# Performance work log

Hardware: AMD Instinct MI355X
Metric: run time of the kernel (lower is better)

Reference implementation:

```python
import jax, jax.numpy as jnp
import numpy as np

H, DH = 16, 64          # num_heads, dim_head
DIM = 1024              # dim_ltn
EPS = 1e-5


def setup_inputs() -> dict:
    key = jax.random.key(0)
    ks = jax.random.split(key, 8)
    b, n_txt, t, m = 2, 2048, 4, 256
    text = jax.random.normal(ks[0], (b, n_txt, DIM), dtype=jnp.float32)
    image = jax.random.normal(ks[1], (b, t, m, DIM), dtype=jnp.float32)
    locations = jax.random.randint(ks[2], (b, n_txt), 0, 2)  # 0/1 media markers
    s = DIM ** -0.5
    Wq = jax.random.normal(ks[3], (DIM, H * DH), dtype=jnp.float32) * s
    Wkv = jax.random.normal(ks[4], (DIM, 2 * H * DH), dtype=jnp.float32) * s
    Wo = jax.random.normal(ks[5], (H * DH, DIM), dtype=jnp.float32) * s
    ln_gamma = jnp.ones((DIM,), dtype=jnp.float32)
    ln_beta = jnp.zeros((DIM,), dtype=jnp.float32)
    return {"text": text, "image": image, "locations": locations,
            "Wq": Wq, "Wkv": Wkv, "Wo": Wo,
            "ln_gamma": ln_gamma, "ln_beta": ln_beta}


def reference(text, image, locations, Wq, Wkv, Wo, ln_gamma, ln_beta):
    scale = DH ** -0.5
    b, t, m, d = image.shape
    # LayerNorm(text)
    mu = text.mean(-1, keepdims=True)
    var = ((text - mu) ** 2).mean(-1, keepdims=True)
    tn = (text - mu) / jnp.sqrt(var + EPS) * ln_gamma + ln_beta
    img = image.reshape(b, t * m, d)             # b (t m) d
    q = tn @ Wq                                  # b n (h dh)
    k, v = jnp.split(img @ Wkv, 2, axis=-1)      # each b tm (h dh)
    split_heads = lambda x: x.reshape(x.shape[0], x.shape[1], H, DH).transpose(0, 2, 1, 3)
    q, k, v = split_heads(q), split_heads(k), split_heads(v)
    attn = jnp.einsum('bhid,bhjd->bhij', q, k) * scale   # b h n (t m)
    txt_time = jnp.cumsum(locations, axis=-1)            # b n : media index per text token
    viz_time = jnp.repeat(jnp.arange(1, t + 1), m)       # (t m)
    # only_attend_to_immediate -> equality mask
    mask = txt_time[:, None, :, None] == viz_time[None, None, None, :]
    neg = -jnp.finfo(attn.dtype).max
    attn = jnp.where(mask, attn, neg)
    attn = jax.nn.softmax(attn, axis=-1)
    # zero attention for text tokens before any media (txt_time == 0)
    attn = jnp.where((txt_time == 0)[:, None, :, None], 0.0, attn)
    out = jnp.einsum('bhij,bhjd->bhid', attn, v)
    out = out.transpose(0, 2, 1, 3).reshape(b, -1, H * DH)
    return out @ Wo
```

## Files before the change

### kernel.cpp

```cpp
#include <hip/hip_runtime.h>

#define BATCH 2
#define NTXT  2048
#define TMED  4
#define MMED  256
#define TM    (TMED * MMED)
#define DIM   1024
#define NH    16
#define DHD   64
#define KVW   2048
#define RMAX  256
#define RT    32

typedef _Float16 f16x8 __attribute__((ext_vector_type(8)));
typedef float    f32x4 __attribute__((ext_vector_type(4)));

__global__ __launch_bounds__(1024) void scan_kernel(const int* __restrict__ loc,
                                                    int* __restrict__ tt,
                                                    int* __restrict__ seg) {
  __shared__ int buf[NTXT];
  __shared__ int s_start, s_end;
  const int b = blockIdx.x;
  const int tid = threadIdx.x;
  if (tid == 0) { s_start = NTXT; s_end = NTXT; }
  buf[tid]        = loc[b * NTXT + tid];
  buf[tid + 1024] = loc[b * NTXT + tid + 1024];
  __syncthreads();
  for (int off = 1; off < NTXT; off <<= 1) {
    int a0 = (tid >= off) ? buf[tid - off] : 0;
    int a1 = buf[tid + 1024 - off];
    __syncthreads();
    buf[tid] += a0;
    buf[tid + 1024] += a1;
    __syncthreads();
  }
  const int v0 = buf[tid], v1 = buf[tid + 1024];
  tt[b * NTXT + tid]        = v0;
  tt[b * NTXT + tid + 1024] = v1;
  if (v0 >= 1) atomicMin(&s_start, tid);
  if (v0 >= 5) atomicMin(&s_end, tid);
  if (v1 >= 1) atomicMin(&s_start, tid + 1024);
  if (v1 >= 5) atomicMin(&s_end, tid + 1024);
  __syncthreads();
  if (tid == 0) {
    seg[b * 2]     = s_start;
    seg[b * 2 + 1] = s_end - s_start;
  }
}

__global__ __launch_bounds__(256) void convert_kernel(const float* __restrict__ Wkv,
                                                      _Float16* __restrict__ Bt) {
  const int tb = blockIdx.x;
  const int k0 = (tb & 15) * 64, n0 = (tb >> 4) * 64;
  __shared__ float tile[64][65];
  const int tid = threadIdx.x;
  const int r = tid >> 4, c4 = (tid & 15) * 4;
#pragma unroll
  for (int i = 0; i < 4; i++) {
    const float4 v = *reinterpret_cast<const float4*>(
        Wkv + (size_t)(k0 + r + i * 16) * KVW + n0 + c4);
    tile[r + i * 16][c4 + 0] = v.x; tile[r + i * 16][c4 + 1] = v.y;
    tile[r + i * 16][c4 + 2] = v.z; tile[r + i * 16][c4 + 3] = v.w;
  }
  __syncthreads();
#pragma unroll
  for (int it = 0; it < 2; it++) {
    const int chunk = it * 256 + tid;
    const int n = chunk >> 3, kc = (chunk & 7) * 8;
    f16x8 h;
#pragma unroll
    for (int j = 0; j < 8; j++) h[j] = (_Float16)tile[kc + j][n];
    *reinterpret_cast<f16x8*>(Bt + (size_t)(n0 + n) * DIM + k0 + kc) = h;
  }
}

__global__ __launch_bounds__(512) void gemm_f16_kernel(
    const float* __restrict__ A, const _Float16* __restrict__ Bt,
    float* __restrict__ C, float* __restrict__ vbar) {
  const int M = BATCH * TM, N = KVW, K = DIM;
  (void)M;
  __shared__ _Float16 As[128 * 32];
  __shared__ _Float16 Bs[128 * 32];
  const int tid = threadIdx.x;
  const int lane = tid & 63, wid = tid >> 6;
  const int wm = wid & 3, wn = wid >> 2;
  const int row0 = blockIdx.y * 128, col0 = blockIdx.x * 128;
  const int srow = tid >> 2, skc = (tid & 3) * 8;
  const int frow = lane & 15, fq = lane >> 4;

  f32x4 acc[2][4] = {};

  for (int k0 = 0; k0 < K; k0 += 32) {
    const float* ap = A + (size_t)(row0 + srow) * K + k0 + skc;
    const float4 a0 = *reinterpret_cast<const float4*>(ap);
    const float4 a1 = *reinterpret_cast<const float4*>(ap + 4);
    f16x8 av;
    av[0] = (_Float16)a0.x; av[1] = (_Float16)a0.y;
    av[2] = (_Float16)a0.z; av[3] = (_Float16)a0.w;
    av[4] = (_Float16)a1.x; av[5] = (_Float16)a1.y;
    av[6] = (_Float16)a1.z; av[7] = (_Float16)a1.w;
    const f16x8 bv = *reinterpret_cast<const f16x8*>(
        Bt + (size_t)(col0 + srow) * K + k0 + skc);
    __syncthreads();
    *reinterpret_cast<f16x8*>(As + tid * 8) = av;
    *reinterpret_cast<f16x8*>(Bs + tid * 8) = bv;
    __syncthreads();

    f16x8 af[2], bf[4];
#pragma unroll
    for (int mt = 0; mt < 2; mt++)
      af[mt] = *reinterpret_cast<const f16x8*>(
          As + (wm * 32 + mt * 16 + frow) * 32 + fq * 8);
#pragma unroll
    for (int nt = 0; nt < 4; nt++)
      bf[nt] = *reinterpret_cast<const f16x8*>(
          Bs + (wn * 64 + nt * 16 + frow) * 32 + fq * 8);
#pragma unroll
    for (int mt = 0; mt < 2; mt++)
#pragma unroll
      for (int nt = 0; nt < 4; nt++)
        acc[mt][nt] = __builtin_amdgcn_mfma_f32_16x16x32_f16(
            af[mt], bf[nt], acc[mt][nt], 0, 0, 0);
  }

#pragma unroll
  for (int mt = 0; mt < 2; mt++)
#pragma unroll
    for (int nt = 0; nt < 4; nt++) {
      const int col = col0 + wn * 64 + nt * 16 + frow;
#pragma unroll
      for (int r = 0; r < 4; r++) {
        const int row = row0 + wm * 32 + mt * 16 + fq * 4 + r;
        C[(size_t)row * N + col] = acc[mt][nt][r];
      }
    }

  if (col0 >= DIM) {
    const int b = row0 >> 10;
#pragma unroll
    for (int nt = 0; nt < 4; nt++) {
      float s = 0.f;
#pragma unroll
      for (int mt = 0; mt < 2; mt++)
#pragma unroll
        for (int r = 0; r < 4; r++) s += acc[mt][nt][r];
      s += __shfl_down(s, 32);
      s += __shfl_down(s, 16);
      if (lane < 16)
        atomicAdd(&vbar[b * DIM + (col0 - DIM) + wn * 64 + nt * 16 + lane],
                  s * (1.0f / (float)TM));
    }
  }
}

__global__ __launch_bounds__(256) void obar_kernel(const float* __restrict__ vbar,
                                                   const float* __restrict__ Wo,
                                                   float* __restrict__ obar) {
  const int be = blockIdx.x;
  const int b = be >> 2, et = be & 3;
  const int ct = blockIdx.y;
  const int tid = threadIdx.x;
  float s = 0.f;
  const float* w = Wo + (size_t)(ct * 128) * DIM + et * 256 + tid;
  const float* vb = vbar + b * DIM + ct * 128;
  for (int c = 0; c < 128; c++) s += vb[c] * w[(size_t)c * DIM];
  atomicAdd(&obar[b * DIM + et * 256 + tid], s);
}

__global__ __launch_bounds__(256) void fill_kernel(
    const float* __restrict__ text, const float* __restrict__ kv,
    const float* __restrict__ Wq, const float* __restrict__ Wo,
    const float* __restrict__ gamma, const float* __restrict__ beta,
    const int* __restrict__ tt, const int* __restrict__ seg,
    const float* __restrict__ obar, float* __restrict__ out) {
  const int tid = threadIdx.x;
  const int b = blockIdx.x >> 11;
  const int i = blockIdx.x & (NTXT - 1);
  const int t = tt[b * NTXT + i];
  float* orow = out + (size_t)(b * NTXT + i) * DIM;

  if (t == 0) {
    for (int c = tid; c < DIM; c += 256) orow[c] = 0.f;
    return;
  }
  if (t > TMED) {
    const float* ob = obar + b * DIM;
    for (int c = tid; c < DIM; c += 256) orow[c] = ob[c];
    return;
  }
  if (i - seg[b * 2] < RMAX) return;

  __shared__ float tn[DIM];
  __shared__ float qrow[DIM];
  __shared__ float oaccs[DIM];
  __shared__ float red[256];
  __shared__ float pbuf[256];
  const float* xrow = text + (size_t)(b * NTXT + i) * DIM;
  float x[4];
  float s = 0.f;
#pragma unroll
  for (int u = 0; u < 4; u++) { x[u] = xrow[tid + 256 * u]; s += x[u]; }
  red[tid] = s; __syncthreads();
  for (int st = 128; st > 0; st >>= 1) {
    if (tid < st) red[tid] += red[tid + st];
    __syncthreads();
  }
  const float mu = red[0] * (1.0f / DIM); __syncthreads();
  float vs = 0.f;
#pragma unroll
  for (int u = 0; u < 4; u++) { float d = x[u] - mu; vs += d * d; }
  red[tid] = vs; __syncthreads();
  for (int st = 128; st > 0; st >>= 1) {
    if (tid < st) red[tid] += red[tid + st];
    __syncthreads();
  }
  const float rstd = rsqrtf(red[0] * (1.0f / DIM) + 1e-5f); __syncthreads();
#pragma unroll
  for (int u = 0; u < 4; u++) {
    const int c = tid + 256 * u;
    tn[c] = (x[u] - mu) * rstd * gamma[c] + beta[c];
  }
  __syncthreads();
  {
    float qa[4] = {0.f, 0.f, 0.f, 0.f};
    for (int c = 0; c < DIM; c++) {
      const float tv = tn[c];
      const float* w = Wq + (size_t)c * DIM + tid;
#pragma unroll
      for (int u = 0; u < 4; u++) qa[u] += tv * w[256 * u];
    }
#pragma unroll
    for (int u = 0; u < 4; u++) qrow[tid + 256 * u] = qa[u];
  }
  __syncthreads();
  const size_t kvrow0 = (size_t)(b * TM + (t - 1) * MMED) * KVW;
  const int d0 = tid & 63, g = tid >> 6;
  for (int h = 0; h < NH; h++) {
    const float* krow = kv + kvrow0 + (size_t)tid * KVW + h * DHD;
    float sc = 0.f;
#pragma unroll
    for (int d = 0; d < DHD; d++) sc += qrow[h * DHD + d] * krow[d];
    sc *= 0.125f;
    red[tid] = sc; __syncthreads();
    for (int st = 128; st > 0; st >>= 1) {
      if (tid < st) red[tid] = fmaxf(red[tid], red[tid + st]);
      __syncthreads();
    }
    const float mx = red[0]; __syncthreads();
    const float e = __expf(sc - mx);
    red[tid] = e; __syncthreads();
    for (int st = 128; st > 0; st >>= 1) {
      if (tid < st) red[tid] += red[tid + st];
      __syncthreads();
    }
    const float inv = 1.0f / red[0]; __syncthreads();
    pbuf[tid] = e * inv; __syncthreads();
    const float* vbase = kv + kvrow0 + (size_t)(g * 64) * KVW + DIM + h * DHD + d0;
    float a = 0.f;
#pragma unroll 8
    for (int j = 0; j < 64; j++) a += pbuf[g * 64 + j] * vbase[(size_t)j * KVW];
    red[tid] = a; __syncthreads();
    if (tid < 64)
      oaccs[h * DHD + tid] = red[tid] + red[64 + tid] + red[128 + tid] + red[192 + tid];
    __syncthreads();
  }
  float oa[4] = {0.f, 0.f, 0.f, 0.f};
  for (int c = 0; c < DIM; c++) {
    const float ov = oaccs[c];
    const float* w = Wo + (size_t)c * DIM + tid;
#pragma unroll
    for (int u = 0; u < 4; u++) oa[u] += ov * w[256 * u];
  }
#pragma unroll
  for (int u = 0; u < 4; u++) orow[tid + 256 * u] = oa[u];
}

__global__ __launch_bounds__(256) void attnh_kernel(
    const float* __restrict__ text, const float* __restrict__ kv,
    const float* __restrict__ Wq, const float* __restrict__ gamma,
    const float* __restrict__ beta, const int* __restrict__ tt,
    const int* __restrict__ seg, float* __restrict__ oacc) {
  const int h = blockIdx.x;
  const int rt = blockIdx.y;
  const int b = blockIdx.z;
  const int i0 = seg[b * 2];
  const int cnt = min(seg[b * 2 + 1], RMAX);
  const int tid = threadIdx.x;
  const int d0 = tid & 63, g = tid >> 6;
  __shared__ float tn_s[DIM];
  __shared__ float q[DHD];
  __shared__ float qp[4][DHD];
  __shared__ float red[256];
  __shared__ float pbuf[256];
  for (int r = rt; r < cnt; r += RT) {
    const int i = i0 + r;
    const int t = tt[b * NTXT + i];
    const float* xrow = text + (size_t)(b * NTXT + i) * DIM;
    float x[4];
    float s = 0.f;
#pragma unroll
    for (int u = 0; u < 4; u++) { x[u] = xrow[tid + 256 * u]; s += x[u]; }
    red[tid] = s; __syncthreads();
    for (int st = 128; st > 0; st >>= 1) {
      if (tid < st) red[tid] += red[tid + st];
      __syncthreads();
    }
    const float mu = red[0] * (1.0f / DIM); __syncthreads();
    float vs = 0.f;
#pragma unroll
    for (int u = 0; u < 4; u++) { float d = x[u] - mu; vs += d * d; }
    red[tid] = vs; __syncthreads();
    for (int st = 128; st > 0; st >>= 1) {
      if (tid < st) red[tid] += red[tid + st];
      __syncthreads();
    }
    const float rstd = rsqrtf(red[0] * (1.0f / DIM) + 1e-5f); __syncthreads();
#pragma unroll
    for (int u = 0; u < 4; u++) {
      const int c = tid + 256 * u;
      tn_s[c] = (x[u] - mu) * rstd * gamma[c] + beta[c];
    }
    __syncthreads();
    float qa = 0.f;
    const float* wq = Wq + (size_t)(g * 256) * DIM + h * DHD + d0;
    for (int c = 0; c < 256; c++) qa += tn_s[g * 256 + c] * wq[(size_t)c * DIM];
    qp[g][d0] = qa; __syncthreads();
    if (tid < 64) q[tid] = qp[0][tid] + qp[1][tid] + qp[2][tid] + qp[3][tid];
    __syncthreads();
    const size_t kvrow0 = (size_t)(b * TM + (t - 1) * MMED) * KVW;
    const float* krow = kv + kvrow0 + (size_t)tid * KVW + h * DHD;
    float sc = 0.f;
#pragma unroll
    for (int d = 0; d < DHD; d += 4) {
      const float4 kk = *reinterpret_cast<const float4*>(&krow[d]);
      sc += q[d] * kk.x + q[d + 1] * kk.y + q[d + 2] * kk.z + q[d + 3] * kk.w;
    }
    sc *= 0.125f;
    red[tid] = sc; __syncthreads();
    for (int st = 128; st > 0; st >>= 1) {
      if (tid < st) red[tid] = fmaxf(red[tid], red[tid + st]);
      __syncthreads();
    }
    const float mx = red[0]; __syncthreads();
    const float e = __expf(sc - mx);
    red[tid] = e; __syncthreads();
    for (int st = 128; st > 0; st >>= 1) {
      if (tid < st) red[tid] += red[tid + st];
      __syncthreads();
    }
    const float inv = 1.0f / red[0]; __syncthreads();
    pbuf[tid] = e * inv; __syncthreads();
    const float* vbase = kv + kvrow0 + (size_t)(g * 64) * KVW + DIM + h * DHD + d0;
    float a = 0.f;
#pragma unroll 8
    for (int j = 0; j < 64; j++) a += pbuf[g * 64 + j] * vbase[(size_t)j * KVW];
    red[tid] = a; __syncthreads();
    if (tid < 64)
      oacc[(size_t)(b * RMAX + r) * DIM + h * DHD + tid] =
          red[tid] + red[64 + tid] + red[128 + tid] + red[192 + tid];
    __syncthreads();
  }
}

__global__ __launch_bounds__(256) void oproj_kernel(
    const float* __restrict__ oacc, const float* __restrict__ Wo,
    const int* __restrict__ seg, float* __restrict__ out) {
  const int ct = blockIdx.x;
  const int rt = blockIdx.y;
  const int b = blockIdx.z;
  const int i0 = seg[b * 2];
  const int cnt = min(seg[b * 2 + 1], RMAX);
  const int tid = threadIdx.x;
  const int d0 = tid & 63, g = tid >> 6;
  __shared__ float op[4][64];
  for (int r = rt; r < cnt; r += RT) {
    const float* arow = oacc + (size_t)(b * RMAX + r) * DIM;
    const float* wo = Wo + (size_t)(g * 256) * DIM + ct * 64 + d0;
    float s = 0.f;
    for (int c = 0; c < 256; c++) s += arow[g * 256 + c] * wo[(size_t)c * DIM];
    op[g][d0] = s; __syncthreads();
    if (tid < 64)
      out[(size_t)(b * NTXT + i0 + r) * DIM + ct * 64 + tid] =
          op[0][tid] + op[1][tid] + op[2][tid] + op[3][tid];
    __syncthreads();
  }
}

extern "C" void kernel_launch(void* const* d_in, const int* in_sizes, int n_in,
                              void* d_out, int out_size, void* d_ws, size_t ws_size,
                              hipStream_t stream) {
  const float* text  = (const float*)d_in[0];
  const float* image = (const float*)d_in[1];
  const int*   loc   = (const int*)d_in[2];
  const float* Wq    = (const float*)d_in[3];
  const float* Wkv   = (const float*)d_in[4];
  const float* Wo    = (const float*)d_in[5];
  const float* gamma = (const float*)d_in[6];
  const float* beta  = (const float*)d_in[7];
  float* out = (float*)d_out;

  float*    kv   = (float*)d_ws;
  _Float16* WkvT = (_Float16*)(kv + (size_t)BATCH * TM * KVW);
  float*    oacc = (float*)WkvT;
  float*    vbar = (float*)(WkvT + (size_t)KVW * DIM);
  float*    obar = vbar + BATCH * DIM;
  int*      tt   = (int*)(obar + BATCH * DIM);
  int*      seg  = tt + BATCH * NTXT;

  scan_kernel<<<BATCH, 1024, 0, stream>>>(loc, tt, seg);
  convert_kernel<<<512, 256, 0, stream>>>(Wkv, WkvT);
  hipMemsetAsync(vbar, 0, 2 * BATCH * DIM * sizeof(float), stream);

  dim3 ggrid(KVW / 128, (BATCH * TM) / 128);
  gemm_f16_kernel<<<ggrid, 512, 0, stream>>>(image, WkvT, kv, vbar);

  obar_kernel<<<dim3(BATCH * 4, 8), 256, 0, stream>>>(vbar, Wo, obar);
  fill_kernel<<<BATCH * NTXT, 256, 0, stream>>>(text, kv, Wq, Wo, gamma, beta,
                                                tt, seg, obar, out);
  attnh_kernel<<<dim3(NH, RT, BATCH), 256, 0, stream>>>(text, kv, Wq, gamma,
                                                        beta, tt, seg, oacc);
  oproj_kernel<<<dim3(16, RT, BATCH), 256, 0, stream>>>(oacc, Wo, seg, out);
}
```

Measured before the change: 178.9 us.

## Merge kernels into five heterogeneous launches, store KV in fp16, precompute q

Replaces the eight-step launch sequence with five kernels that each carry several independent jobs, selected by block index: scan plus image-mean, weight transpose plus LayerNorm plus vbar, then GEMM plus q projection plus obar, then fill plus attention. The K/V projection output is now written as fp16, which halves the workspace traffic for the GEMM output and the attention reads. vbar is computed from the image mean times Wkv instead of through atomics in the GEMM epilogue. The aim is to cut launch gaps and memory traffic, at the cost of extra fp16 rounding in K/V and some idle or imbalanced blocks in the mixed-role kernels.

```diff
diff --git a/kernel.cpp b/kernel.cpp
--- a/kernel.cpp
+++ b/kernel.cpp
@@ -15,286 +15,260 @@
 typedef _Float16 f16x8 __attribute__((ext_vector_type(8)));
 typedef float    f32x4 __attribute__((ext_vector_type(4)));
 
-__global__ __launch_bounds__(1024) void scan_kernel(const int* __restrict__ loc,
-                                                    int* __restrict__ tt,
-                                                    int* __restrict__ seg) {
+__global__ __launch_bounds__(1024) void k1_scan_ibar(
+    const int* __restrict__ loc, const float* __restrict__ image,
+    int* __restrict__ tt, int* __restrict__ seg, float* __restrict__ ibar) {
   __shared__ int buf[NTXT];
   __shared__ int s_start, s_end;
-  const int b = blockIdx.x;
+  const int idx = blockIdx.x;
   const int tid = threadIdx.x;
-  if (tid == 0) { s_start = NTXT; s_end = NTXT; }
-  buf[tid]        = loc[b * NTXT + tid];
-  buf[tid + 1024] = loc[b * NTXT + tid + 1024];
-  __syncthreads();
-  for (int off = 1; off < NTXT; off <<= 1) {
-    int a0 = (tid >= off) ? buf[tid - off] : 0;
-    int a1 = buf[tid + 1024 - off];
-    __syncthreads();
-    buf[tid] += a0;
-    buf[tid + 1024] += a1;
-    __syncthreads();
+  if (idx < BATCH) {
+    const int b = idx;
+    if (tid == 0) { s_start = NTXT; s_end = NTXT; }
+    buf[tid]        = loc[b * NTXT + tid];
+    buf[tid + 1024] = loc[b * NTXT + tid + 1024];
+    __syncthreads();
+    for (int off = 1; off < NTXT; off <<= 1) {
+      int a0 = (tid >= off) ? buf[tid - off] : 0;
+      int a1 = buf[tid + 1024 - off];
+      __syncthreads();
+      buf[tid] += a0;
+      buf[tid + 1024] += a1;
+      __syncthreads();
+    }
+    const int v0 = buf[tid], v1 = buf[tid + 1024];
+    tt[b * NTXT + tid]        = v0;
+    tt[b * NTXT + tid + 1024] = v1;
+    if (v0 >= 1) atomicMin(&s_start, tid);
+    if (v0 >= 5) atomicMin(&s_end, tid);
+    if (v1 >= 1) atomicMin(&s_start, tid + 1024);
+    if (v1 >= 5) atomicMin(&s_end, tid + 1024);
+    __syncthreads();
+    if (tid == 0) {
+      seg[b * 2]     = s_start;
+      seg[b * 2 + 1] = s_end - s_start;
+    }
+  } else {
+    const int j = idx - BATCH;
+    const int b = j >> 3, rt = j & 7;
+    const float* p = image + (size_t)(b * TM + rt * 128) * DIM + tid;
+    float s = 0.f;
+#pragma unroll 4
+    for (int r = 0; r < 128; r++) s += p[(size_t)r * DIM];
+    atomicAdd(&ibar[b * DIM + tid], s * (1.0f / (float)TM));
   }
-  const int v0 = buf[tid], v1 = buf[tid + 1024];
-  tt[b * NTXT + tid]        = v0;
-  tt[b * NTXT + tid + 1024] = v1;
-  if (v0 >= 1) atomicMin(&s_start, tid);
-  if (v0 >= 5) atomicMin(&s_end, tid);
-  if (v1 >= 1) atomicMin(&s_start, tid + 1024);
-  if (v1 >= 5) atomicMin(&s_end, tid + 1024);
-  __syncthreads();
-  if (tid == 0) {
-    seg[b * 2]     = s_start;
-    seg[b * 2 + 1] = s_end - s_start;
+}
+
+__global__ __launch_bounds__(256) void k2_prep(
+    const float* __restrict__ Wkv, const float* __restrict__ text,
+    const float* __restrict__ gamma, const float* __restrict__ beta,
+    const int* __restrict__ seg, const float* __restrict__ ibar,
+    _Float16* __restrict__ WkvT, float* __restrict__ tn,
+    float* __restrict__ vbar) {
+  __shared__ float tile[64][65];
+  __shared__ float red[256];
+  const int idx = blockIdx.x;
+  const int tid = threadIdx.x;
+  if (idx < 512) {
+    const int k0 = (idx & 15) * 64, n0 = (idx >> 4) * 64;
+    const int r = tid >> 4, c4 = (tid & 15) * 4;
+#pragma unroll
+    for (int i = 0; i < 4; i++) {
+      const float4 v = *reinterpret_cast<const float4*>(
+          Wkv + (size_t)(k0 + r + i * 16) * KVW + n0 + c4);
+      tile[r + i * 16][c4 + 0] = v.x; tile[r + i * 16][c4 + 1] = v.y;
+      tile[r + i * 16][c4 + 2] = v.z; tile[r + i * 16][c4 + 3] = v.w;
+    }
+    __syncthreads();
+#pragma unroll
+    for (int it = 0; it < 2; it++) {
+      const int chunk = it * 256 + tid;
+      const int n = chunk >> 3, kc = (chunk & 7) * 8;
+      f16x8 h;
+#pragma unroll
+      for (int j = 0; j < 8; j++) h[j] = (_Float16)tile[kc + j][n];
+      *reinterpret_cast<f16x8*>(WkvT + (size_t)(n0 + n) * DIM + k0 + kc) = h;
+    }
+  } else if (idx < 576) {
+    const int j = idx - 512;
+    const int b = j >> 5, rt = j & 31;
+    const int i0 = seg[b * 2];
+    const int cnt = min(seg[b * 2 + 1], RMAX);
+    for (int r = rt; r < cnt; r += RT) {
+      const float* xrow = text + (size_t)(b * NTXT + i0 + r) * DIM;
+      float x[4];
+      float s = 0.f;
+#pragma unroll
+      for (int u = 0; u < 4; u++) { x[u] = xrow[tid + 256 * u]; s += x[u]; }
+      red[tid] = s; __syncthreads();
+      for (int st = 128; st > 0; st >>= 1) {
+        if (tid < st) red[tid] += red[tid + st];
+        __syncthreads();
+      }
+      const float mu = red[0] * (1.0f / DIM); __syncthreads();
+      float vs = 0.f;
+#pragma unroll
+      for (int u = 0; u < 4; u++) { float d = x[u] - mu; vs += d * d; }
+      red[tid] = vs; __syncthreads();
+      for (int st = 128; st > 0; st >>= 1) {
+        if (tid < st) red[tid] += red[tid + st];
+        __syncthreads();
+      }
+      const float rstd = rsqrtf(red[0] * (1.0f / DIM) + 1e-5f); __syncthreads();
+      float* trow = tn + (size_t)(b * RMAX + r) * DIM;
+#pragma unroll
+      for (int u = 0; u < 4; u++) {
+        const int c = tid + 256 * u;
+        trow[c] = (x[u] - mu) * rstd * gamma[c] + beta[c];
+      }
+      __syncthreads();
+    }
+  } else {
+    const int j = idx - 576;
+    const int b = j >> 2, et = j & 3;
+    const int e = et * 256 + tid;
+    const float* vb = ibar + b * DIM;
+    float s = 0.f;
+    for (int c = 0; c < DIM; c++) s += vb[c] * Wkv[(size_t)c * KVW + DIM + e];
+    vbar[b * DIM + e] = s;
   }
 }
 
-__global__ __launch_bounds__(256) void convert_kernel(const float* __restrict__ Wkv,
-                                                      _Float16* __restrict__ Bt) {
-  const int tb = blockIdx.x;
-  const int k0 = (tb & 15) * 64, n0 = (tb >> 4) * 64;
-  __shared__ float tile[64][65];
+__global__ __launch_bounds__(512) void k3_gemm_qproj_obar(
+    const float* __restrict__ image, const _Float16* __restrict__ WkvT,
+    const float* __restrict__ Wq, const float* __restrict__ Wo,
+    const float* __restrict__ tn, const float* __restrict__ vbar,
+    const int* __restrict__ seg, _Float16* __restrict__ kv16,
+    float* __restrict__ qbuf, float* __restrict__ obar) {
+  __shared__ char smem[49152];
+  const int idx = blockIdx.x;
   const int tid = threadIdx.x;
-  const int r = tid >> 4, c4 = (tid & 15) * 4;
-#pragma unroll
-  for (int i = 0; i < 4; i++) {
-    const float4 v = *reinterpret_cast<const float4*>(
-        Wkv + (size_t)(k0 + r + i * 16) * KVW + n0 + c4);
-    tile[r + i * 16][c4 + 0] = v.x; tile[r + i * 16][c4 + 1] = v.y;
-    tile[r + i * 16][c4 + 2] = v.z; tile[r + i * 16][c4 + 3] = v.w;
+  if (idx < 256) {
+    _Float16* As = (_Float16*)smem;
+    _Float16* Bs = As + 128 * 32;
+    const int lane = tid & 63, wid = tid >> 6;
+    const int wm = wid & 3, wn = wid >> 2;
+    const int row0 = (idx >> 4) * 128, col0 = (idx & 15) * 128;
+    const int srow = tid >> 2, skc = (tid & 3) * 8;
+    const int frow = lane & 15, fq = lane >> 4;
+    f32x4 acc[2][4] = {};
+    for (int k0 = 0; k0 < DIM; k0 += 32) {
+      const float* ap = image + (size_t)(row0 + srow) * DIM + k0 + skc;
+      const float4 a0 = *reinterpret_cast<const float4*>(ap);
+      const float4 a1 = *reinterpret_cast<const float4*>(ap + 4);
+      f16x8 av;
+      av[0] = (_Float16)a0.x; av[1] = (_Float16)a0.y;
+      av[2] = (_Float16)a0.z; av[3] = (_Float16)a0.w;
+      av[4] = (_Float16)a1.x; av[5] = (_Float16)a1.y;
+      av[6] = (_Float16)a1.z; av[7] = (_Float16)a1.w;
+      const f16x8 bv = *reinterpret_cast<const f16x8*>(
+          WkvT + (size_t)(col0 + srow) * DIM + k0 + skc);
+      __syncthreads();
+      *reinterpret_cast<f16x8*>(As + tid * 8) = av;
+      *reinterpret_cast<f16x8*>(Bs + tid * 8) = bv;
+      __syncthreads();
+      f16x8 af[2], bf[4];
+#pragma unroll
+      for (int mt = 0; mt < 2; mt++)
+        af[mt] = *reinterpret_cast<const f16x8*>(
+            As + (wm * 32 + mt * 16 + frow) * 32 + fq * 8);
+#pragma unroll
+      for (int nt = 0; nt < 4; nt++)
+        bf[nt] = *reinterpret_cast<const f16x8*>(
+            Bs + (wn * 64 + nt * 16 + frow) * 32 + fq * 8);
+#pragma unroll
+      for (int mt = 0; mt < 2; mt++)
+#pragma unroll
+        for (int nt = 0; nt < 4; nt++)
+          acc[mt][nt] = __builtin_amdgcn_mfma_f32_16x16x32_f16(
+              af[mt], bf[nt], acc[mt][nt], 0, 0, 0);
+    }
+#pragma unroll
+    for (int mt = 0; mt < 2; mt++)
+#pragma unroll
+      for (int nt = 0; nt < 4; nt++) {
+        const int col = col0 + wn * 64 + nt * 16 + frow;
+#pragma unroll
+        for (int r = 0; r < 4; r++) {
+          const int row = row0 + wm * 32 + mt * 16 + fq * 4 + r;
+          kv16[(size_t)row * KVW + col] = (_Float16)acc[mt][nt][r];
+        }
+      }
+  } else if (idx < 272) {
+    float* tn_s = (float*)smem;
+    float* qred = tn_s + 8 * 1024;
+    const int j = idx - 256;
+    const int b = j >> 3, nt = j & 7;
+    const int n0 = nt * 128;
+    const int d0 = tid & 127, g = tid >> 7;
+    const int cnt = min(seg[b * 2 + 1], RMAX);
+    for (int r0 = 0; r0 < cnt; r0 += 8) {
+      const float* src = tn + (size_t)(b * RMAX + r0) * DIM;
+      for (int i = tid; i < 8 * 1024; i += 512) tn_s[i] = src[i];
+      __syncthreads();
+      float acc[8] = {};
+      const float* wq = Wq + (size_t)(g * 256) * DIM + n0 + d0;
+      for (int c = 0; c < 256; c++) {
+        const float w = wq[(size_t)c * DIM];
+#pragma unroll
+        for (int rr = 0; rr < 8; rr++)
+          acc[rr] += tn_s[rr * 1024 + g * 256 + c] * w;
+      }
+#pragma unroll
+      for (int rr = 0; rr < 8; rr++) qred[(g * 8 + rr) * 128 + d0] = acc[rr];
+      __syncthreads();
+      if (g == 0) {
+#pragma unroll
+        for (int rr = 0; rr < 8; rr++) {
+          if (r0 + rr < cnt) {
+            const float s = qred[rr * 128 + d0] + qred[(8 + rr) * 128 + d0] +
+                            qred[(16 + rr) * 128 + d0] + qred[(24 + rr) * 128 + d0];
+            qbuf[(size_t)(b * RMAX + r0 + rr) * DIM + n0 + d0] = s;
+          }
+        }
+      }
+      __syncthreads();
+    }
+  } else {
+    const int j = idx - 272;
+    const int b = j >> 1, et = j & 1;
+    const int e = et * 512 + tid;
+    const float* vb = vbar + b * DIM;
+    float s = 0.f;
+    for (int c = 0; c < DIM; c++) s += vb[c] * Wo[(size_t)c * DIM + e];
+    obar[b * DIM + e] = s;
   }
-  __syncthreads();
-#pragma unroll
-  for (int it = 0; it < 2; it++) {
-    const int chunk = it * 256 + tid;
-    const int n = chunk >> 3, kc = (chunk & 7) * 8;
-    f16x8 h;
-#pragma unroll
-    for (int j = 0; j < 8; j++) h[j] = (_Float16)tile[kc + j][n];
-    *reinterpret_cast<f16x8*>(Bt + (size_t)(n0 + n) * DIM + k0 + kc) = h;
-  }
-}
-
-__global__ __launch_bounds__(512) void gemm_f16_kernel(
-    const float* __restrict__ A, const _Float16* __restrict__ Bt,
-    float* __restrict__ C, float* __restrict__ vbar) {
-  const int M = BATCH * TM, N = KVW, K = DIM;
-  (void)M;
-  __shared__ _Float16 As[128 * 32];
-  __shared__ _Float16 Bs[128 * 32];
-  const int tid = threadIdx.x;
-  const int lane = tid & 63, wid = tid >> 6;
-  const int wm = wid & 3, wn = wid >> 2;
-  const int row0 = blockIdx.y * 128, col0 = blockIdx.x * 128;
-  const int srow = tid >> 2, skc = (tid & 3) * 8;
-  const int frow = lane & 15, fq = lane >> 4;
-
-  f32x4 acc[2][4] = {};
-
-  for (int k0 = 0; k0 < K; k0 += 32) {
-    const float* ap = A + (size_t)(row0 + srow) * K + k0 + skc;
-    const float4 a0 = *reinterpret_cast<const float4*>(ap);
-    const float4 a1 = *reinterpret_cast<const float4*>(ap + 4);
-    f16x8 av;
-    av[0] = (_Float16)a0.x; av[1] = (_Float16)a0.y;
-    av[2] = (_Float16)a0.z; av[3] = (_Float16)a0.w;
-    av[4] = (_Float16)a1.x; av[5] = (_Float16)a1.y;
-    av[6] = (_Float16)a1.z; av[7] = (_Float16)a1.w;
-    const f16x8 bv = *reinterpret_cast<const f16x8*>(
-        Bt + (size_t)(col0 + srow) * K + k0 + skc);
-    __syncthreads();
-    *reinterpret_cast<f16x8*>(As + tid * 8) = av;
-    *reinterpret_cast<f16x8*>(Bs + tid * 8) = bv;
-    __syncthreads();
-
-    f16x8 af[2], bf[4];
-#pragma unroll
-    for (int mt = 0; mt < 2; mt++)
-      af[mt] = *reinterpret_cast<const f16x8*>(
-          As + (wm * 32 + mt * 16 + frow) * 32 + fq * 8);
-#pragma unroll
-    for (int nt = 0; nt < 4; nt++)
-      bf[nt] = *reinterpret_cast<const f16x8*>(
-          Bs + (wn * 64 + nt * 16 + frow) * 32 + fq * 8);
-#pragma unroll
-    for (int mt = 0; mt < 2; mt++)
-#pragma unroll
-      for (int nt = 0; nt < 4; nt++)
-        acc[mt][nt] = __builtin_amdgcn_mfma_f32_16x16x32_f16(
-            af[mt], bf[nt], acc[mt][nt], 0, 0, 0);
-  }
-
-#pragma unroll
-  for (int mt = 0; mt < 2; mt++)
-#pragma unroll
-    for (int nt = 0; nt < 4; nt++) {
-      const int col = col0 + wn * 64 + nt * 16 + frow;
-#pragma unroll
-      for (int r = 0; r < 4; r++) {
-        const int row = row0 + wm * 32 + mt * 16 + fq * 4 + r;
-        C[(size_t)row * N + col] = acc[mt][nt][r];
-      }
-    }
-
-  if (col0 >= DIM) {
-    const int b = row0 >> 10;
-#pragma unroll
-    for (int nt = 0; nt < 4; nt++) {
-      float s = 0.f;
-#pragma unroll
-      for (int mt = 0; mt < 2; mt++)
-#pragma unroll
-        for (int r = 0; r < 4; r++) s += acc[mt][nt][r];
-      s += __shfl_down(s, 32);
-      s += __shfl_down(s, 16);
-      if (lane < 16)
-        atomicAdd(&vbar[b * DIM + (col0 - DIM) + wn * 64 + nt * 16 + lane],
-                  s * (1.0f / (float)TM));
-    }
-  }
-}
-
-__global__ __launch_bounds__(256) void obar_kernel(const float* __restrict__ vbar,
-                                                   const float* __restrict__ Wo,
-                                                   float* __restrict__ obar) {
-  const int be = blockIdx.x;
-  const int b = be >> 2, et = be & 3;
-  const int ct = blockIdx.y;
-  const int tid = threadIdx.x;
-  float s = 0.f;
-  const float* w = Wo + (size_t)(ct * 128) * DIM + et * 256 + tid;
-  const float* vb = vbar + b * DIM + ct * 128;
-  for (int c = 0; c < 128; c++) s += vb[c] * w[(size_t)c * DIM];
-  atomicAdd(&obar[b * DIM + et * 256 + tid], s);
-}
-
-__global__ __launch_bounds__(256) void fill_kernel(
-    const float* __restrict__ text, const float* __restrict__ kv,
+}
+
+__global__ __launch_bounds__(256) void k4_fill_attn(
+    const float* __restrict__ text, const _Float16* __restrict__ kv16,
     const float* __restrict__ Wq, const float* __restrict__ Wo,
     const float* __restrict__ gamma, const float* __restrict__ beta,
     const int* __restrict__ tt, const int* __restrict__ seg,
-    const float* __restrict__ obar, float* __restrict__ out) {
-  const int tid = threadIdx.x;
-  const int b = blockIdx.x >> 11;
-  const int i = blockIdx.x & (NTXT - 1);
-  const int t = tt[b * NTXT + i];
-  float* orow = out + (size_t)(b * NTXT + i) * DIM;
-
-  if (t == 0) {
-    for (int c = tid; c < DIM; c += 256) orow[c] = 0.f;
-    return;
-  }
-  if (t > TMED) {
-    const float* ob = obar + b * DIM;
-    for (int c = tid; c < DIM; c += 256) orow[c] = ob[c];
-    return;
-  }
-  if (i - seg[b * 2] < RMAX) return;
-
-  __shared__ float tn[DIM];
-  __shared__ float qrow[DIM];
-  __shared__ float oaccs[DIM];
+    const float* __restrict__ obar, const float* __restrict__ qbuf,
+    float* __restrict__ oacc, float* __restrict__ out) {
   __shared__ float red[256];
   __shared__ float pbuf[256];
-  const float* xrow = text + (size_t)(b * NTXT + i) * DIM;
-  float x[4];
-  float s = 0.f;
-#pragma unroll
-  for (int u = 0; u < 4; u++) { x[u] = xrow[tid + 256 * u]; s += x[u]; }
-  red[tid] = s; __syncthreads();
-  for (int st = 128; st > 0; st >>= 1) {
-    if (tid < st) red[tid] += red[tid + st];
-    __syncthreads();
-  }
-  const float mu = red[0] * (1.0f / DIM); __syncthreads();
-  float vs = 0.f;
-#pragma unroll
-  for (int u = 0; u < 4; u++) { float d = x[u] - mu; vs += d * d; }
-  red[tid] = vs; __syncthreads();
-  for (int st = 128; st > 0; st >>= 1) {
-    if (tid < st) red[tid] += red[tid + st];
-    __syncthreads();
-  }
-  const float rstd = rsqrtf(red[0] * (1.0f / DIM) + 1e-5f); __syncthreads();
-#pragma unroll
-  for (int u = 0; u < 4; u++) {
-    const int c = tid + 256 * u;
-    tn[c] = (x[u] - mu) * rstd * gamma[c] + beta[c];
-  }
-  __syncthreads();
-  {
-    float qa[4] = {0.f, 0.f, 0.f, 0.f};
-    for (int c = 0; c < DIM; c++) {
-      const float tv = tn[c];
-      const float* w = Wq + (size_t)c * DIM + tid;
-#pragma unroll
-      for (int u = 0; u < 4; u++) qa[u] += tv * w[256 * u];
-    }
-#pragma unroll
-    for (int u = 0; u < 4; u++) qrow[tid + 256 * u] = qa[u];
-  }
-  __syncthreads();
-  const size_t kvrow0 = (size_t)(b * TM + (t - 1) * MMED) * KVW;
-  const int d0 = tid & 63, g = tid >> 6;
-  for (int h = 0; h < NH; h++) {
-    const float* krow = kv + kvrow0 + (size_t)tid * KVW + h * DHD;
-    float sc = 0.f;
-#pragma unroll
-    for (int d = 0; d < DHD; d++) sc += qrow[h * DHD + d] * krow[d];
-    sc *= 0.125f;
-    red[tid] = sc; __syncthreads();
-    for (int st = 128; st > 0; st >>= 1) {
-      if (tid < st) red[tid] = fmaxf(red[tid], red[tid + st]);
-      __syncthreads();
-    }
-    const float mx = red[0]; __syncthreads();
-    const float e = __expf(sc - mx);
-    red[tid] = e; __syncthreads();
-    for (int st = 128; st > 0; st >>= 1) {
-      if (tid < st) red[tid] += red[tid + st];
-      __syncthreads();
-    }
-    const float inv = 1.0f / red[0]; __syncthreads();
-    pbuf[tid] = e * inv; __syncthreads();
-    const float* vbase = kv + kvrow0 + (size_t)(g * 64) * KVW + DIM + h * DHD + d0;
-    float a = 0.f;
-#pragma unroll 8
-    for (int j = 0; j < 64; j++) a += pbuf[g * 64 + j] * vbase[(size_t)j * KVW];
-    red[tid] = a; __syncthreads();
-    if (tid < 64)
-      oaccs[h * DHD + tid] = red[tid] + red[64 + tid] + red[128 + tid] + red[192 + tid];
-    __syncthreads();
-  }
-  float oa[4] = {0.f, 0.f, 0.f, 0.f};
-  for (int c = 0; c < DIM; c++) {
-    const float ov = oaccs[c];
-    const float* w = Wo + (size_t)c * DIM + tid;
-#pragma unroll
-    for (int u = 0; u < 4; u++) oa[u] += ov * w[256 * u];
-  }
-#pragma unroll
-  for (int u = 0; u < 4; u++) orow[tid + 256 * u] = oa[u];
-}
-
-__global__ __launch_bounds__(256) void attnh_kernel(
-    const float* __restrict__ text, const float* __restrict__ kv,
-    const float* __restrict__ Wq, const float* __restrict__ gamma,
-    const float* __restrict__ beta, const int* __restrict__ tt,
-    const int* __restrict__ seg, float* __restrict__ oacc) {
-  const int h = blockIdx.x;
-  const int rt = blockIdx.y;
-  const int b = blockIdx.z;
-  const int i0 = seg[b * 2];
-  const int cnt = min(seg[b * 2 + 1], RMAX);
+  const int idx = blockIdx.x;
   const int tid = threadIdx.x;
-  const int d0 = tid & 63, g = tid >> 6;
-  __shared__ float tn_s[DIM];
-  __shared__ float q[DHD];
-  __shared__ float qp[4][DHD];
-  __shared__ float red[256];
-  __shared__ float pbuf[256];
-  for (int r = rt; r < cnt; r += RT) {
-    const int i = i0 + r;
+  if (idx < BATCH * NTXT) {
+    const int b = idx >> 11;
+    const int i = idx & (NTXT - 1);
     const int t = tt[b * NTXT + i];
+    float* orow = out + (size_t)(b * NTXT + i) * DIM;
+    if (t == 0) {
+      for (int c = tid; c < DIM; c += 256) orow[c] = 0.f;
+      return;
+    }
+    if (t > TMED) {
+      const float* ob = obar + b * DIM;
+      for (int c = tid; c < DIM; c += 256) orow[c] = ob[c];
+      return;
+    }
+    if (i - seg[b * 2] < RMAX) return;
+    __shared__ float tns[DIM];
+    __shared__ float qrow[DIM];
+    __shared__ float oaccs[DIM];
     const float* xrow = text + (size_t)(b * NTXT + i) * DIM;
     float x[4];
     float s = 0.f;
@@ -318,51 +292,111 @@
 #pragma unroll
     for (int u = 0; u < 4; u++) {
       const int c = tid + 256 * u;
-      tn_s[c] = (x[u] - mu) * rstd * gamma[c] + beta[c];
-    }
-    __syncthreads();
-    float qa = 0.f;
-    const float* wq = Wq + (size_t)(g * 256) * DIM + h * DHD + d0;
-    for (int c = 0; c < 256; c++) qa += tn_s[g * 256 + c] * wq[(size_t)c * DIM];
-    qp[g][d0] = qa; __syncthreads();
-    if (tid < 64) q[tid] = qp[0][tid] + qp[1][tid] + qp[2][tid] + qp[3][tid];
+      tns[c] = (x[u] - mu) * rstd * gamma[c] + beta[c];
+    }
+    __syncthreads();
+    {
+      float qa[4] = {0.f, 0.f, 0.f, 0.f};
+      for (int c = 0; c < DIM; c++) {
+        const float tv = tns[c];
+        const float* w = Wq + (size_t)c * DIM + tid;
+#pragma unroll
+        for (int u = 0; u < 4; u++) qa[u] += tv * w[256 * u];
+      }
+#pragma unroll
+      for (int u = 0; u < 4; u++) qrow[tid + 256 * u] = qa[u];
+    }
     __syncthreads();
     const size_t kvrow0 = (size_t)(b * TM + (t - 1) * MMED) * KVW;
-    const float* krow = kv + kvrow0 + (size_t)tid * KVW + h * DHD;
-    float sc = 0.f;
-#pragma unroll
-    for (int d = 0; d < DHD; d += 4) {
-      const float4 kk = *reinterpret_cast<const float4*>(&krow[d]);
-      sc += q[d] * kk.x + q[d + 1] * kk.y + q[d + 2] * kk.z + q[d + 3] * kk.w;
-    }
-    sc *= 0.125f;
-    red[tid] = sc; __syncthreads();
-    for (int st = 128; st > 0; st >>= 1) {
-      if (tid < st) red[tid] = fmaxf(red[tid], red[tid + st]);
-      __syncthreads();
-    }
-    const float mx = red[0]; __syncthreads();
-    const float e = __expf(sc - mx);
-    red[tid] = e; __syncthreads();
-    for (int st = 128; st > 0; st >>= 1) {
-      if (tid < st) red[tid] += red[tid + st];
-      __syncthreads();
-    }
-    const float inv = 1.0f / red[0]; __syncthreads();
-    pbuf[tid] = e * inv; __syncthreads();
-    const float* vbase = kv + kvrow0 + (size_t)(g * 64) * KVW + DIM + h * DHD + d0;
-    float a = 0.f;
+    const int d0 = tid & 63, g = tid >> 6;
+    for (int h = 0; h < NH; h++) {
+      const _Float16* krow = kv16 + kvrow0 + (size_t)tid * KVW + h * DHD;
+      float sc = 0.f;
+#pragma unroll
+      for (int d = 0; d < DHD; d++) sc += qrow[h * DHD + d] * (float)krow[d];
+      sc *= 0.125f;
+      red[tid] = sc; __syncthreads();
+      for (int st = 128; st > 0; st >>= 1) {
+        if (tid < st) red[tid] = fmaxf(red[tid], red[tid + st]);
+        __syncthreads();
+      }
+      const float mx = red[0]; __syncthreads();
+      const float e = __expf(sc - mx);
+      red[tid] = e; __syncthreads();
+      for (int st = 128; st > 0; st >>= 1) {
+        if (tid < st) red[tid] += red[tid + st];
+        __syncthreads();
+      }
+      const float inv = 1.0f / red[0]; __syncthreads();
+      pbuf[tid] = e * inv; __syncthreads();
+      const _Float16* vbase = kv16 + kvrow0 + (size_t)(g * 64) * KVW + DIM + h * DHD + d0;
+      float a = 0.f;
 #pragma unroll 8
-    for (int j = 0; j < 64; j++) a += pbuf[g * 64 + j] * vbase[(size_t)j * KVW];
-    red[tid] = a; __syncthreads();
-    if (tid < 64)
-      oacc[(size_t)(b * RMAX + r) * DIM + h * DHD + tid] =
-          red[tid] + red[64 + tid] + red[128 + tid] + red[192 + tid];
-    __syncthreads();
+      for (int jj = 0; jj < 64; jj++) a += pbuf[g * 64 + jj] * (float)vbase[(size_t)jj * KVW];
+      red[tid] = a; __syncthreads();
+      if (tid < 64)
+        oaccs[h * DHD + tid] = red[tid] + red[64 + tid] + red[128 + tid] + red[192 + tid];
+      __syncthreads();
+    }
+    float oa[4] = {0.f, 0.f, 0.f, 0.f};
+    for (int c = 0; c < DIM; c++) {
+      const float ov = oaccs[c];
+      const float* w = Wo + (size_t)c * DIM + tid;
+#pragma unroll
+      for (int u = 0; u < 4; u++) oa[u] += ov * w[256 * u];
+    }
+#pragma unroll
+    for (int u = 0; u < 4; u++) orow[tid + 256 * u] = oa[u];
+  } else {
+    __shared__ float qs[DHD];
+    const int j = idx - BATCH * NTXT;
+    const int h = j & 15, rt = (j >> 4) & 31, b = j >> 9;
+    const int i0 = seg[b * 2];
+    const int cnt = min(seg[b * 2 + 1], RMAX);
+    const int d0 = tid & 63, g = tid >> 6;
+    for (int r = rt; r < cnt; r += RT) {
+      const int i = i0 + r;
+      const int t = tt[b * NTXT + i];
+      if (tid < 64) qs[tid] = qbuf[(size_t)(b * RMAX + r) * DIM + h * DHD + tid];
+      __syncthreads();
+      const size_t kvrow0 = (size_t)(b * TM + (t - 1) * MMED) * KVW;
+      const _Float16* krow = kv16 + kvrow0 + (size_t)tid * KVW + h * DHD;
+      float sc = 0.f;
+#pragma unroll
+      for (int d = 0; d < DHD; d += 8) {
+        const f16x8 kk = *reinterpret_cast<const f16x8*>(krow + d);
+#pragma unroll
+        for (int u = 0; u < 8; u++) sc += qs[d + u] * (float)kk[u];
+      }
+      sc *= 0.125f;
+      red[tid] = sc; __syncthreads();
+      for (int st = 128; st > 0; st >>= 1) {
+        if (tid < st) red[tid] = fmaxf(red[tid], red[tid + st]);
+        __syncthreads();
+      }
+      const float mx = red[0]; __syncthreads();
+      const float e = __expf(sc - mx);
+      red[tid] = e; __syncthreads();
+      for (int st = 128; st > 0; st >>= 1) {
+        if (tid < st) red[tid] += red[tid + st];
+        __syncthreads();
+      }
+      const float inv = 1.0f / red[0]; __syncthreads();
+      pbuf[tid] = e * inv; __syncthreads();
+      const _Float16* vbase = kv16 + kvrow0 + (size_t)(g * 64) * KVW + DIM + h * DHD + d0;
+      float a = 0.f;
+#pragma unroll 8
+      for (int jj = 0; jj < 64; jj++) a += pbuf[g * 64 + jj] * (float)vbase[(size_t)jj * KVW];
+      red[tid] = a; __syncthreads();
+      if (tid < 64)
+        oacc[(size_t)(b * RMAX + r) * DIM + h * DHD + tid] =
+            red[tid] + red[64 + tid] + red[128 + tid] + red[192 + tid];
+      __syncthreads();
+    }
   }
 }
 
-__global__ __launch_bounds__(256) void oproj_kernel(
+__global__ __launch_bounds__(256) void k5_oproj(
     const float* __restrict__ oacc, const float* __restrict__ Wo,
     const int* __restrict__ seg, float* __restrict__ out) {
   const int ct = blockIdx.x;
@@ -399,25 +433,24 @@
   const float* beta  = (const float*)d_in[7];
   float* out = (float*)d_out;
 
-  float*    kv   = (float*)d_ws;
-  _Float16* WkvT = (_Float16*)(kv + (size_t)BATCH * TM * KVW);
+  _Float16* kv16 = (_Float16*)d_ws;
+  _Float16* WkvT = kv16 + (size_t)BATCH * TM * KVW;
   float*    oacc = (float*)WkvT;
-  float*    vbar = (float*)(WkvT + (size_t)KVW * DIM);
+  float*    tn   = (float*)(WkvT + (size_t)KVW * DIM);
+  float*    qbuf = tn + (size_t)BATCH * RMAX * DIM;
+  float*    ibar = qbuf + (size_t)BATCH * RMAX * DIM;
+  float*    vbar = ibar + BATCH * DIM;
   float*    obar = vbar + BATCH * DIM;
   int*      tt   = (int*)(obar + BATCH * DIM);
   int*      seg  = tt + BATCH * NTXT;
 
-  scan_kernel<<<BATCH, 1024, 0, stream>>>(loc, tt, seg);
-  convert_kernel<<<512, 256, 0, stream>>>(Wkv, WkvT);
-  hipMemsetAsync(vbar, 0, 2 * BATCH * DIM * sizeof(float), stream);
-
-  dim3 ggrid(KVW / 128, (BATCH * TM) / 128);
-  gemm_f16_kernel<<<ggrid, 512, 0, stream>>>(image, WkvT, kv, vbar);
-
-  obar_kernel<<<dim3(BATCH * 4, 8), 256, 0, stream>>>(vbar, Wo, obar);
-  fill_kernel<<<BATCH * NTXT, 256, 0, stream>>>(text, kv, Wq, Wo, gamma, beta,
-                                                tt, seg, obar, out);
-  attnh_kernel<<<dim3(NH, RT, BATCH), 256, 0, stream>>>(text, kv, Wq, gamma,
-                                                        beta, tt, seg, oacc);
-  oproj_kernel<<<dim3(16, RT, BATCH), 256, 0, stream>>>(oacc, Wo, seg, out);
-}
+  hipMemsetAsync(ibar, 0, BATCH * DIM * sizeof(float), stream);
+  k1_scan_ibar<<<BATCH + 16, 1024, 0, stream>>>(loc, image, tt, seg, ibar);
+  k2_prep<<<584, 256, 0, stream>>>(Wkv, text, gamma, beta, seg, ibar,
+                                   WkvT, tn, vbar);
+  k3_gemm_qproj_obar<<<276, 512, 0, stream>>>(image, WkvT, Wq, Wo, tn, vbar,
+                                              seg, kv16, qbuf, obar);
+  k4_fill_attn<<<BATCH * NTXT + NH * RT * BATCH, 256, 0, stream>>>(
+      text, kv16, Wq, Wo, gamma, beta, tt, seg, obar, qbuf, oacc, out);
+  k5_oproj<<<dim3(16, RT, BATCH), 256, 0, stream>>>(oacc, Wo, seg, out);
+}
```

Result: slower. 226.4 us (+26.5%).
